# Performance work log

Hardware: AMD Instinct MI355X
Metric: run time of the kernel (lower is better)

The kernel has to match this reference:

```python
import jax, jax.numpy as jnp
import numpy as np

DIM = 512
EPS = 1e-08
LN_EPS = 1e-05  # torch LayerNorm default


def layer_norm(x, g, b):
    mu = jnp.mean(x, axis=-1, keepdims=True)
    var = jnp.mean(jnp.square(x - mu), axis=-1, keepdims=True)
    return (x - mu) * jax.lax.rsqrt(var + LN_EPS) * g + b


def setup_inputs() -> dict:
    key = jax.random.key(0)
    ks = jax.random.split(key, 10)
    B, NQ, NK, D = 8, 1024, 2048, DIM
    s = 1.0 / np.sqrt(D)
    return {
        "inputs": jax.random.normal(ks[0], (B, NQ, D), jnp.float32),
        "context": jax.random.normal(ks[1], (B, NK, D), jnp.float32),
        "ln_in_g": jnp.ones((D,), jnp.float32),
        "ln_in_b": jnp.zeros((D,), jnp.float32),
        "ln_ctx_g": jnp.ones((D,), jnp.float32),
        "ln_ctx_b": jnp.zeros((D,), jnp.float32),
        "Wq": jax.random.uniform(ks[2], (D, D), jnp.float32, -s, s),
        "bq": jax.random.uniform(ks[3], (D,), jnp.float32, -s, s),
        "Wk": jax.random.uniform(ks[4], (D, D), jnp.float32, -s, s),
        "bk": jax.random.uniform(ks[5], (D,), jnp.float32, -s, s),
        "Wv": jax.random.uniform(ks[6], (D, D), jnp.float32, -s, s),
        "bv": jax.random.uniform(ks[7], (D,), jnp.float32, -s, s),
    }


def reference(inputs, context, ln_in_g, ln_in_b, ln_ctx_g, ln_ctx_b, Wq, bq, Wk, bk, Wv, bv):
    x = layer_norm(inputs, ln_in_g, ln_in_b)
    c = layer_norm(context, ln_ctx_g, ln_ctx_b)
    q = x @ Wq.T + bq  # [B, Nq, D]
    k = c @ Wk.T + bk  # [B, Nk, D]
    v = c @ Wv.T + bv  # [B, Nk, D]
    scale = DIM ** (-0.5)
    dots = jnp.einsum('bid,bjd->bij', q, k) * scale  # [B, Nq, Nk]
    attn = jax.nn.softmax(dots, axis=1) + EPS  # softmax over query axis
    attn = attn / jnp.sum(attn, axis=2, keepdims=True)  # renorm over key axis
    updates = jnp.einsum('bjd,bij->bid', v, attn)
    return updates
```

## Files before the change

kernel.cpp:

```cpp
#include <hip/hip_runtime.h>

using u16 = unsigned short;
typedef __attribute__((ext_vector_type(8))) short short8;
typedef __attribute__((ext_vector_type(4))) float floatx4;

#define NQ 1024
#define NK 2048
#define DD 512

__device__ __forceinline__ u16 f2bf(float f) {
  union { float f; unsigned u; } x; x.f = f;
  unsigned r = (x.u + 0x7fffu + ((x.u >> 16) & 1u)) >> 16;
  return (u16)r;
}
__device__ __forceinline__ float bf2f(u16 u) {
  union { unsigned u; float f; } x; x.u = ((unsigned)u) << 16; return x.f;
}
__device__ __forceinline__ float wave_sum(float v) {
#pragma unroll
  for (int off = 32; off > 0; off >>= 1) v += __shfl_down(v, off, 64);
  return v;
}
__device__ __forceinline__ void gload16(const u16* g, const u16* l) {
  __builtin_amdgcn_global_load_lds(
      (const __attribute__((address_space(1))) void*)g,
      (__attribute__((address_space(3))) void*)l, 16, 0, 0);
}

__global__ __launch_bounds__(256) void ln_prep(
    const float* __restrict__ X1, const float* __restrict__ G1,
    const float* __restrict__ B1, u16* __restrict__ Y1,
    const float* __restrict__ X2, const float* __restrict__ G2,
    const float* __restrict__ B2, u16* __restrict__ Y2,
    const float* __restrict__ Wq, const float* __restrict__ Wk,
    const float* __restrict__ Wv, u16* __restrict__ wqb,
    u16* __restrict__ wkb, u16* __restrict__ wvb, float* __restrict__ Zero) {
  int row = blockIdx.x;
  const int t = threadIdx.x;
  if (row >= 24576) {
    int bx = row - 24576;
    if (bx < 768) {
      const float* src = bx < 256 ? Wq : (bx < 512 ? Wk : Wv);
      u16* dst = bx < 256 ? wqb : (bx < 512 ? wkb : wvb);
      int i = ((bx & 255) * 256 + t) * 4;
      float4 v = *(const float4*)(src + i);
      ushort4 o;
      o.x = f2bf(v.x); o.y = f2bf(v.y); o.z = f2bf(v.z); o.w = f2bf(v.w);
      *(ushort4*)(dst + i) = o;
    } else {
      int i = ((bx - 768) * 256 + t) * 4;
      float4 z = {0.f, 0.f, 0.f, 0.f};
      *(float4*)(Zero + i) = z;
    }
    return;
  }
  const float *X, *G, *Bv; u16* Y;
  if (row < 8192) { X = X1; G = G1; Bv = B1; Y = Y1; }
  else { row -= 8192; X = X2; G = G2; Bv = B2; Y = Y2; }
  const float2 v = ((const float2*)(X + (long)row * DD))[t];
  float s = v.x + v.y, ss = v.x * v.x + v.y * v.y;
  __shared__ float red[8];
  float a = wave_sum(s), b = wave_sum(ss);
  if ((t & 63) == 0) { red[t >> 6] = a; red[4 + (t >> 6)] = b; }
  __syncthreads();
  float tot = red[0] + red[1] + red[2] + red[3];
  float tss = red[4] + red[5] + red[6] + red[7];
  float mu = tot * (1.f / DD);
  float var = tss * (1.f / DD) - mu * mu;
  float rs = rsqrtf(var + 1e-5f);
  float2 g2 = ((const float2*)G)[t];
  float2 b2 = ((const float2*)Bv)[t];
  ushort2 o;
  o.x = f2bf((v.x - mu) * rs * g2.x + b2.x);
  o.y = f2bf((v.y - mu) * rs * g2.y + b2.y);
  ((ushort2*)(Y + (long)row * DD))[t] = o;
}

__global__ __launch_bounds__(256) void gemm_bt(
    const u16* A, const u16* B, const float* bias, void* Cout,
    const u16* A2, const u16* B2, const float* bias2, void* Cout2,
    int K, long sAb, long sBb, long sCb, int ldC,
    float scale, int epi, float* aux0, const float* aux1) {
  __shared__ u16 lA[128 * 32];
  __shared__ u16 lB[128 * 32];
  __shared__ float colred[128];

  int m0, n0, bz;
  if (epi == 3) {
    bz = blockIdx.x; m0 = blockIdx.z * 128; n0 = blockIdx.y * 128;
  } else {
    bz = blockIdx.z; m0 = blockIdx.x * 128; n0 = blockIdx.y * 128;
    if (A2 != nullptr && blockIdx.x >= 64) {
      A = A2; B = B2; bias = bias2; Cout = Cout2;
      m0 = (blockIdx.x - 64) * 128;
    }
  }
  A += (long)bz * sAb;
  B += (long)bz * sBb;
  const int t = threadIdx.x, wave = t >> 6, lane = t & 63;
  const int fm = lane & 15, fq = lane >> 4;
  const int wm = (wave >> 1) * 64, wn = (wave & 1) * 64;

  const u16* gA = A + (long)(m0 + wave * 16 + (lane >> 2)) * K + (lane & 3) * 8;
  const u16* gB = B + (long)(n0 + wave * 16 + (lane >> 2)) * K + (lane & 3) * 8;
  const long g64 = (long)64 * K;
  u16* lAw0 = lA + (wave * 16) * 32;
  u16* lAw1 = lA + (64 + wave * 16) * 32;
  u16* lBw0 = lB + (wave * 16) * 32;
  u16* lBw1 = lB + (64 + wave * 16) * 32;

  floatx4 acc[4][4];
#pragma unroll
  for (int x = 0; x < 4; ++x)
#pragma unroll
    for (int y = 0; y < 4; ++y) { floatx4 z = {0.f, 0.f, 0.f, 0.f}; acc[x][y] = z; }

  const int nkt = K >> 5;
  for (int kt = 0; kt < nkt; ++kt) {
    gload16(gA, lAw0);
    gload16(gA + g64, lAw1);
    gload16(gB, lBw0);
    gload16(gB + g64, lBw1);
    gA += 32; gB += 32;
    __syncthreads();
    short8 af[4], bfr[4];
#pragma unroll
    for (int x = 0; x < 4; ++x)
      af[x] = *(const short8*)&lA[(wm + x * 16 + fm) * 32 + fq * 8];
#pragma unroll
    for (int y = 0; y < 4; ++y)
      bfr[y] = *(const short8*)&lB[(wn + y * 16 + fm) * 32 + fq * 8];
#pragma unroll
    for (int x = 0; x < 4; ++x)
#pragma unroll
      for (int y = 0; y < 4; ++y)
        acc[x][y] = __builtin_amdgcn_mfma_f32_16x16x32_bf16(af[x], bfr[y], acc[x][y], 0, 0, 0);
    __syncthreads();
  }

  if (epi == 0) {
    float bs[4];
#pragma unroll
    for (int y = 0; y < 4; ++y) bs[y] = bias[n0 + wn + y * 16 + fm];
#pragma unroll
    for (int x = 0; x < 4; ++x)
#pragma unroll
      for (int y = 0; y < 4; ++y)
#pragma unroll
        for (int r = 0; r < 4; ++r) {
          int row = m0 + wm + x * 16 + fq * 4 + r;
          int col = n0 + wn + y * 16 + fm;
          ((u16*)Cout)[(long)bz * sCb + (long)row * ldC + col] =
              f2bf(acc[x][y][r] + bs[y]);
        }
  } else if (epi == 3) {
    float s4[4] = {0.f, 0.f, 0.f, 0.f};
#pragma unroll
    for (int x = 0; x < 4; ++x)
#pragma unroll
      for (int y = 0; y < 4; ++y)
#pragma unroll
        for (int r = 0; r < 4; ++r) {
          int row = m0 + wm + x * 16 + fq * 4 + r;
          int col = n0 + wn + y * 16 + fm;
          float e = __expf(acc[x][y][r] * scale);
          s4[y] += e;
          ((u16*)Cout)[(long)bz * sCb + (long)row * ldC + col] = f2bf(e);
        }
#pragma unroll
    for (int y = 0; y < 4; ++y) {
      s4[y] += __shfl_xor(s4[y], 16, 64);
      s4[y] += __shfl_xor(s4[y], 32, 64);
    }
    if (t < 128) colred[t] = 0.f;
    __syncthreads();
    if (fq == 0) {
#pragma unroll
      for (int y = 0; y < 4; ++y) atomicAdd(&colred[wn + y * 16 + fm], s4[y]);
    }
    __syncthreads();
    if (t < 128) atomicAdd(&aux0[bz * 2048 + n0 + t], colred[t]);
  } else {
    const int bb = n0 >> 11;
    const int j0c = n0 & 2047;
    float bsr[4][4];
#pragma unroll
    for (int x = 0; x < 4; ++x)
#pragma unroll
      for (int r = 0; r < 4; ++r)
        bsr[x][r] = bias[m0 + wm + x * 16 + fq * 4 + r];
    float izv[4];
#pragma unroll
    for (int y = 0; y < 4; ++y)
      izv[y] = __builtin_amdgcn_rcpf(aux1[bb * 2048 + j0c + wn + y * 16 + fm]);
    u16* Cg = (u16*)Cout + (long)bb * (512L * 2048) + j0c;
    float rs[4][4];
#pragma unroll
    for (int x = 0; x < 4; ++x)
#pragma unroll
      for (int r = 0; r < 4; ++r) rs[x][r] = 0.f;
#pragma unroll
    for (int x = 0; x < 4; ++x)
#pragma unroll
      for (int y = 0; y < 4; ++y)
#pragma unroll
        for (int r = 0; r < 4; ++r) {
          int rowd = m0 + wm + x * 16 + fq * 4 + r;
          int col = wn + y * 16 + fm;
          float val = acc[x][y][r] + bsr[x][r];
          rs[x][r] += val;
          Cg[(long)rowd * 2048 + col] = f2bf(val * izv[y]);
        }
#pragma unroll
    for (int x = 0; x < 4; ++x)
#pragma unroll
      for (int r = 0; r < 4; ++r) {
        float s = rs[x][r];
        s += __shfl_xor(s, 1, 64);
        s += __shfl_xor(s, 2, 64);
        s += __shfl_xor(s, 4, 64);
        s += __shfl_xor(s, 8, 64);
        if (fm == 0)
          atomicAdd(&aux0[bb * 512 + m0 + wm + x * 16 + fq * 4 + r], s);
      }
  }
}

__global__ __launch_bounds__(256) void rowsumR(const u16* __restrict__ E,
    const float* __restrict__ Z, float* __restrict__ invR) {
  const int row = blockIdx.x;
  const int b = row >> 10;
  const u16* p = E + (long)row * NK;
  const float* zp = Z + b * NK;
  const int t = threadIdx.x, j0 = t * 8;
  short8 v = *(const short8*)(p + j0);
  float4 z0 = *(const float4*)(zp + j0);
  float4 z1 = *(const float4*)(zp + j0 + 4);
  float sum = bf2f((u16)v[0]) * __builtin_amdgcn_rcpf(z0.x) +
              bf2f((u16)v[1]) * __builtin_amdgcn_rcpf(z0.y) +
              bf2f((u16)v[2]) * __builtin_amdgcn_rcpf(z0.z) +
              bf2f((u16)v[3]) * __builtin_amdgcn_rcpf(z0.w) +
              bf2f((u16)v[4]) * __builtin_amdgcn_rcpf(z1.x) +
              bf2f((u16)v[5]) * __builtin_amdgcn_rcpf(z1.y) +
              bf2f((u16)v[6]) * __builtin_amdgcn_rcpf(z1.z) +
              bf2f((u16)v[7]) * __builtin_amdgcn_rcpf(z1.w);
  __shared__ float red[4];
  float a = wave_sum(sum);
  if ((t & 63) == 0) red[t >> 6] = a;
  __syncthreads();
  if (t == 0) {
    float R = red[0] + red[1] + red[2] + red[3] + 2048.f * 1e-8f;
    invR[row] = 1.0f / R;
  }
}

__global__ __launch_bounds__(256) void gemm_pv(const u16* __restrict__ E,
    const u16* __restrict__ V, const float* __restrict__ colV,
    const float* __restrict__ invR, float* __restrict__ out) {
  __shared__ u16 lds[6144];
  u16* lA = lds;
  u16* lB = lds + 2048;
  float* sO = (float*)lds;
  const int b = blockIdx.z;
  const int m0 = blockIdx.x * 64, n0 = blockIdx.y * 128;
  const int t = threadIdx.x, wave = t >> 6, lane = t & 63;
  const int fm = lane & 15, fq = lane >> 4;
  const int wml = (wave >> 1) * 32, wnl = (wave & 1) * 64;

  const u16* gA = E + (long)b * (1024L * 2048) +
                  (long)(m0 + wave * 16 + (lane >> 2)) * 2048 + (lane & 3) * 8;
  const u16* gB = V + (long)b * (512L * 2048) +
                  (long)(n0 + wave * 16 + (lane >> 2)) * 2048 + (lane & 3) * 8;
  u16* lAw = lA + (wave * 16) * 32;
  u16* lBw0 = lB + (wave * 16) * 32;
  u16* lBw1 = lB + (64 + wave * 16) * 32;

  floatx4 acc[2][4];
#pragma unroll
  for (int x = 0; x < 2; ++x)
#pragma unroll
    for (int y = 0; y < 4; ++y) { floatx4 z = {0.f, 0.f, 0.f, 0.f}; acc[x][y] = z; }

  for (int kt = 0; kt < 64; ++kt) {
    gload16(gA, lAw);
    gload16(gB, lBw0);
    gload16(gB + 64L * 2048, lBw1);
    gA += 32; gB += 32;
    __syncthreads();
    short8 af[2], bfr[4];
#pragma unroll
    for (int x = 0; x < 2; ++x)
      af[x] = *(const short8*)&lA[(wml + x * 16 + fm) * 32 + fq * 8];
#pragma unroll
    for (int y = 0; y < 4; ++y)
      bfr[y] = *(const short8*)&lB[(wnl + y * 16 + fm) * 32 + fq * 8];
#pragma unroll
    for (int x = 0; x < 2; ++x)
#pragma unroll
      for (int y = 0; y < 4; ++y)
        acc[x][y] = __builtin_amdgcn_mfma_f32_16x16x32_bf16(af[x], bfr[y], acc[x][y], 0, 0, 0);
    __syncthreads();
  }

  float cv[4], ir[8];
#pragma unroll
  for (int y = 0; y < 4; ++y) cv[y] = colV[b * 512 + n0 + wnl + y * 16 + fm];
#pragma unroll
  for (int x = 0; x < 2; ++x)
#pragma unroll
    for (int r = 0; r < 4; ++r)
      ir[x * 4 + r] = invR[b * 1024 + m0 + wml + x * 16 + fq * 4 + r];

  float* og = out + (long)b * (1024L * 512) + n0;
#pragma unroll
  for (int c = 0; c < 4; ++c) {
    __syncthreads();
    if (wml == (c >> 1) * 32) {
      int x = c & 1;
#pragma unroll
      for (int y = 0; y < 4; ++y)
#pragma unroll
        for (int r = 0; r < 4; ++r)
          sO[(fq * 4 + r) * 132 + wnl + y * 16 + fm] =
              (acc[x][y][r] + 1e-8f * cv[y]) * ir[x * 4 + r];
    }
    __syncthreads();
    int row = t >> 4, colc = (t & 15) * 8;
    float4 v0 = *(const float4*)&sO[row * 132 + colc];
    float4 v1 = *(const float4*)&sO[row * 132 + colc + 4];
    float* op = og + (long)(m0 + c * 16 + row) * 512 + colc;
    *(float4*)op = v0;
    *(float4*)(op + 4) = v1;
  }
}

extern "C" void kernel_launch(void* const* d_in, const int* in_sizes, int n_in,
                              void* d_out, int out_size, void* d_ws, size_t ws_size,
                              hipStream_t stream) {
  const float* inputs  = (const float*)d_in[0];
  const float* context = (const float*)d_in[1];
  const float* ln_in_g = (const float*)d_in[2];
  const float* ln_in_b = (const float*)d_in[3];
  const float* ln_ctx_g = (const float*)d_in[4];
  const float* ln_ctx_b = (const float*)d_in[5];
  const float* Wq = (const float*)d_in[6];
  const float* bq = (const float*)d_in[7];
  const float* Wk = (const float*)d_in[8];
  const float* bk = (const float*)d_in[9];
  const float* Wv = (const float*)d_in[10];
  const float* bv = (const float*)d_in[11];
  float* out = (float*)d_out;

  u16* ws = (u16*)d_ws;
  u16* xb  = ws;
  u16* qb  = xb + 8192L * 512;
  u16* cb  = qb + 8192L * 512;
  u16* wqb = cb + 16384L * 512;
  u16* wkb = wqb + 512L * 512;
  u16* wvb = wkb + 512L * 512;
  u16* kb  = wvb + 512L * 512;
  u16* vTs = kb + 16384L * 512;
  u16* E   = vTs + 8L * 512 * 2048;
  float* Z    = (float*)(E + 8L * 1024 * 2048);
  float* colV = Z + 8L * 2048;
  float* invR = colV + 8L * 512;

  const float scale = 0.04419417382415922f;

  ln_prep<<<25364, 256, 0, stream>>>(inputs, ln_in_g, ln_in_b, xb,
                                     context, ln_ctx_g, ln_ctx_b, cb,
                                     Wq, Wk, Wv, wqb, wkb, wvb, Z);
  gemm_bt<<<dim3(192, 4, 1), 256, 0, stream>>>(xb, wqb, bq, qb,
      cb, wkb, bk, kb, 512, 0L, 0L, 0L, 512, 1.0f, 0, nullptr, nullptr);
  gemm_bt<<<dim3(8, 16, 8), 256, 0, stream>>>(qb, kb, nullptr, E,
      nullptr, nullptr, nullptr, nullptr,
      512, 1024L * 512, 2048L * 512, 1024L * 2048, 2048, scale, 3, Z, nullptr);
  gemm_bt<<<dim3(4, 128, 1), 256, 0, stream>>>(wvb, cb, bv, vTs,
      nullptr, nullptr, nullptr, nullptr,
      512, 0L, 0L, 0L, 2048, 1.0f, 6, colV, Z);
  rowsumR<<<8192, 256, 0, stream>>>(E, Z, invR);
  gemm_pv<<<dim3(16, 4, 8), 256, 0, stream>>>(E, vTs, colV, invR, out);
}
```

Measured before the change: 253.9 us.

## Double K-tile depth to 64 with XOR-swizzled LDS and smaller PV tiles

Both GEMM kernels now stage 64-wide K slices per iteration instead of 32, with an XOR swizzle on LDS column chunks so fragment reads avoid bank conflicts. This halves the number of barrier pairs per K loop. The PV kernel shrinks its output tile from 64x128 to 64x64, doubling the grid, and writes results straight to global memory instead of staging them through LDS. In exchange, LDS use per block grows in gemm_bt, and the direct epilogue writes are less coalesced.

Result: faster. 230.5 us (-9.2%).

```diff
diff --git a/kernel.cpp b/kernel.cpp
--- a/kernel.cpp
+++ b/kernel.cpp
@@ -81,8 +81,8 @@
     const u16* A2, const u16* B2, const float* bias2, void* Cout2,
     int K, long sAb, long sBb, long sCb, int ldC,
     float scale, int epi, float* aux0, const float* aux1) {
-  __shared__ u16 lA[128 * 32];
-  __shared__ u16 lB[128 * 32];
+  __shared__ u16 lA[128 * 64];
+  __shared__ u16 lB[128 * 64];
   __shared__ float colred[128];
 
   int m0, n0, bz;
@@ -101,13 +101,13 @@
   const int fm = lane & 15, fq = lane >> 4;
   const int wm = (wave >> 1) * 64, wn = (wave & 1) * 64;
 
-  const u16* gA = A + (long)(m0 + wave * 16 + (lane >> 2)) * K + (lane & 3) * 8;
-  const u16* gB = B + (long)(n0 + wave * 16 + (lane >> 2)) * K + (lane & 3) * 8;
-  const long g64 = (long)64 * K;
-  u16* lAw0 = lA + (wave * 16) * 32;
-  u16* lAw1 = lA + (64 + wave * 16) * 32;
-  u16* lBw0 = lB + (wave * 16) * 32;
-  u16* lBw1 = lB + (64 + wave * 16) * 32;
+  const int srow = t >> 3;
+  const int swz = ((t & 7) ^ (srow & 7)) * 8;
+  const u16* gA = A + (long)(m0 + srow) * K + swz;
+  const u16* gB = B + (long)(n0 + srow) * K + swz;
+  const long gk32 = 32L * K;
+  u16* dA = lA + wave * 512;
+  u16* dB = lB + wave * 512;
 
   floatx4 acc[4][4];
 #pragma unroll
@@ -115,26 +115,34 @@
 #pragma unroll
     for (int y = 0; y < 4; ++y) { floatx4 z = {0.f, 0.f, 0.f, 0.f}; acc[x][y] = z; }
 
-  const int nkt = K >> 5;
+  const int nkt = K >> 6;
   for (int kt = 0; kt < nkt; ++kt) {
-    gload16(gA, lAw0);
-    gload16(gA + g64, lAw1);
-    gload16(gB, lBw0);
-    gload16(gB + g64, lBw1);
-    gA += 32; gB += 32;
-    __syncthreads();
-    short8 af[4], bfr[4];
-#pragma unroll
-    for (int x = 0; x < 4; ++x)
-      af[x] = *(const short8*)&lA[(wm + x * 16 + fm) * 32 + fq * 8];
-#pragma unroll
-    for (int y = 0; y < 4; ++y)
-      bfr[y] = *(const short8*)&lB[(wn + y * 16 + fm) * 32 + fq * 8];
-#pragma unroll
-    for (int x = 0; x < 4; ++x)
+    gload16(gA, dA);
+    gload16(gA + gk32, dA + 2048);
+    gload16(gA + 2 * gk32, dA + 4096);
+    gload16(gA + 3 * gk32, dA + 6144);
+    gload16(gB, dB);
+    gload16(gB + gk32, dB + 2048);
+    gload16(gB + 2 * gk32, dB + 4096);
+    gload16(gB + 3 * gk32, dB + 6144);
+    gA += 64; gB += 64;
+    __syncthreads();
+#pragma unroll
+    for (int ks = 0; ks < 2; ++ks) {
+      short8 af[4], bfr[4];
+      const int csl = ((ks * 4 + fq) ^ (fm & 7)) * 8;
+#pragma unroll
+      for (int x = 0; x < 4; ++x)
+        af[x] = *(const short8*)&lA[(wm + x * 16 + fm) * 64 + csl];
 #pragma unroll
       for (int y = 0; y < 4; ++y)
-        acc[x][y] = __builtin_amdgcn_mfma_f32_16x16x32_bf16(af[x], bfr[y], acc[x][y], 0, 0, 0);
+        bfr[y] = *(const short8*)&lB[(wn + y * 16 + fm) * 64 + csl];
+#pragma unroll
+      for (int x = 0; x < 4; ++x)
+#pragma unroll
+        for (int y = 0; y < 4; ++y)
+          acc[x][y] = __builtin_amdgcn_mfma_f32_16x16x32_bf16(af[x], bfr[y], acc[x][y], 0, 0, 0);
+    }
     __syncthreads();
   }
 
@@ -257,81 +265,73 @@
 __global__ __launch_bounds__(256) void gemm_pv(const u16* __restrict__ E,
     const u16* __restrict__ V, const float* __restrict__ colV,
     const float* __restrict__ invR, float* __restrict__ out) {
-  __shared__ u16 lds[6144];
-  u16* lA = lds;
-  u16* lB = lds + 2048;
-  float* sO = (float*)lds;
+  __shared__ u16 lA[64 * 64];
+  __shared__ u16 lB[64 * 64];
   const int b = blockIdx.z;
-  const int m0 = blockIdx.x * 64, n0 = blockIdx.y * 128;
+  const int m0 = blockIdx.x * 64, n0 = blockIdx.y * 64;
   const int t = threadIdx.x, wave = t >> 6, lane = t & 63;
   const int fm = lane & 15, fq = lane >> 4;
-  const int wml = (wave >> 1) * 32, wnl = (wave & 1) * 64;
-
-  const u16* gA = E + (long)b * (1024L * 2048) +
-                  (long)(m0 + wave * 16 + (lane >> 2)) * 2048 + (lane & 3) * 8;
-  const u16* gB = V + (long)b * (512L * 2048) +
-                  (long)(n0 + wave * 16 + (lane >> 2)) * 2048 + (lane & 3) * 8;
-  u16* lAw = lA + (wave * 16) * 32;
-  u16* lBw0 = lB + (wave * 16) * 32;
-  u16* lBw1 = lB + (64 + wave * 16) * 32;
-
-  floatx4 acc[2][4];
+  const int wm = (wave >> 1) * 32, wn = (wave & 1) * 32;
+
+  const int srow = t >> 3;
+  const int swz = ((t & 7) ^ (srow & 7)) * 8;
+  const u16* gA = E + (long)b * (1024L * 2048) + (long)(m0 + srow) * 2048 + swz;
+  const u16* gB = V + (long)b * (512L * 2048) + (long)(n0 + srow) * 2048 + swz;
+  u16* dA = lA + wave * 512;
+  u16* dB = lB + wave * 512;
+
+  floatx4 acc[2][2];
 #pragma unroll
   for (int x = 0; x < 2; ++x)
 #pragma unroll
-    for (int y = 0; y < 4; ++y) { floatx4 z = {0.f, 0.f, 0.f, 0.f}; acc[x][y] = z; }
-
-  for (int kt = 0; kt < 64; ++kt) {
-    gload16(gA, lAw);
-    gload16(gB, lBw0);
-    gload16(gB + 64L * 2048, lBw1);
-    gA += 32; gB += 32;
-    __syncthreads();
-    short8 af[2], bfr[4];
-#pragma unroll
-    for (int x = 0; x < 2; ++x)
-      af[x] = *(const short8*)&lA[(wml + x * 16 + fm) * 32 + fq * 8];
-#pragma unroll
-    for (int y = 0; y < 4; ++y)
-      bfr[y] = *(const short8*)&lB[(wnl + y * 16 + fm) * 32 + fq * 8];
-#pragma unroll
-    for (int x = 0; x < 2; ++x)
-#pragma unroll
-      for (int y = 0; y < 4; ++y)
-        acc[x][y] = __builtin_amdgcn_mfma_f32_16x16x32_bf16(af[x], bfr[y], acc[x][y], 0, 0, 0);
-    __syncthreads();
-  }
-
-  float cv[4], ir[8];
-#pragma unroll
-  for (int y = 0; y < 4; ++y) cv[y] = colV[b * 512 + n0 + wnl + y * 16 + fm];
+    for (int y = 0; y < 2; ++y) { floatx4 z = {0.f, 0.f, 0.f, 0.f}; acc[x][y] = z; }
+
+  for (int kt = 0; kt < 32; ++kt) {
+    gload16(gA, dA);
+    gload16(gA + 32L * 2048, dA + 2048);
+    gload16(gB, dB);
+    gload16(gB + 32L * 2048, dB + 2048);
+    gA += 64; gB += 64;
+    __syncthreads();
+#pragma unroll
+    for (int ks = 0; ks < 2; ++ks) {
+      short8 af[2], bfr[2];
+      const int csl = ((ks * 4 + fq) ^ (fm & 7)) * 8;
+#pragma unroll
+      for (int x = 0; x < 2; ++x)
+        af[x] = *(const short8*)&lA[(wm + x * 16 + fm) * 64 + csl];
+#pragma unroll
+      for (int y = 0; y < 2; ++y)
+        bfr[y] = *(const short8*)&lB[(wn + y * 16 + fm) * 64 + csl];
+#pragma unroll
+      for (int x = 0; x < 2; ++x)
+#pragma unroll
+        for (int y = 0; y < 2; ++y)
+          acc[x][y] = __builtin_amdgcn_mfma_f32_16x16x32_bf16(af[x], bfr[y], acc[x][y], 0, 0, 0);
+    }
+    __syncthreads();
+  }
+
+  float cv[2], ir[8];
+#pragma unroll
+  for (int y = 0; y < 2; ++y) cv[y] = colV[b * 512 + n0 + wn + y * 16 + fm];
 #pragma unroll
   for (int x = 0; x < 2; ++x)
 #pragma unroll
     for (int r = 0; r < 4; ++r)
-      ir[x * 4 + r] = invR[b * 1024 + m0 + wml + x * 16 + fq * 4 + r];
-
-  float* og = out + (long)b * (1024L * 512) + n0;
-#pragma unroll
-  for (int c = 0; c < 4; ++c) {
-    __syncthreads();
-    if (wml == (c >> 1) * 32) {
-      int x = c & 1;
-#pragma unroll
-      for (int y = 0; y < 4; ++y)
-#pragma unroll
-        for (int r = 0; r < 4; ++r)
-          sO[(fq * 4 + r) * 132 + wnl + y * 16 + fm] =
-              (acc[x][y][r] + 1e-8f * cv[y]) * ir[x * 4 + r];
-    }
-    __syncthreads();
-    int row = t >> 4, colc = (t & 15) * 8;
-    float4 v0 = *(const float4*)&sO[row * 132 + colc];
-    float4 v1 = *(const float4*)&sO[row * 132 + colc + 4];
-    float* op = og + (long)(m0 + c * 16 + row) * 512 + colc;
-    *(float4*)op = v0;
-    *(float4*)(op + 4) = v1;
-  }
+      ir[x * 4 + r] = invR[b * 1024 + m0 + wm + x * 16 + fq * 4 + r];
+  float* og = out + (long)b * (1024L * 512);
+#pragma unroll
+  for (int x = 0; x < 2; ++x)
+#pragma unroll
+    for (int y = 0; y < 2; ++y)
+#pragma unroll
+      for (int r = 0; r < 4; ++r) {
+        int row = m0 + wm + x * 16 + fq * 4 + r;
+        int col = n0 + wn + y * 16 + fm;
+        og[(long)row * 512 + col] =
+            (acc[x][y][r] + 1e-8f * cv[y]) * ir[x * 4 + r];
+      }
 }
 
 extern "C" void kernel_launch(void* const* d_in, const int* in_sizes, int n_in,
@@ -379,5 +379,5 @@
       nullptr, nullptr, nullptr, nullptr,
       512, 0L, 0L, 0L, 2048, 1.0f, 6, colV, Z);
   rowsumR<<<8192, 256, 0, stream>>>(E, Z, invR);
-  gemm_pv<<<dim3(16, 4, 8), 256, 0, stream>>>(E, vTs, colV, invR, out);
-}
+  gemm_pv<<<dim3(16, 8, 8), 256, 0, stream>>>(E, vTs, colV, invR, out);
+}
```
